# Kernel tuning notes

Hardware: AMD Instinct MI355X
Metric: run time of the kernel (lower is better)

Reference implementation:

```python
import jax, jax.numpy as jnp
import numpy as np


def setup_inputs() -> dict:
    key = jax.random.key(0)
    ks = jax.random.split(key, 4)
    B, T, D, H = 64, 512, 512, 1024
    return {
        "x": jax.random.normal(ks[0], (B, T, D), dtype=jnp.float32),
        "kz": jax.random.normal(ks[1], (D, H), dtype=jnp.float32) * (1.0 / np.sqrt(D)),
        "kr": jax.random.normal(ks[2], (D, H), dtype=jnp.float32) * (1.0 / np.sqrt(D)),
        "kh": jax.random.normal(ks[3], (D, H), dtype=jnp.float32) * (1.0 / np.sqrt(D)),
        "mz": jnp.ones((H,), dtype=jnp.float32),
        "mr": jnp.ones((H,), dtype=jnp.float32),
        "br": jnp.zeros((H,), dtype=jnp.float32),
        "bz": jnp.zeros((H,), dtype=jnp.float32),
    }


def reference(x, kz, kr, kh, mz, mr, br, bz):
    B, T, D = x.shape
    H = kz.shape[1]
    # Precompute input projections for all timesteps (batched GEMMs),
    # identical math to per-step matmuls in the original cell.
    xz = jnp.einsum("btd,dh->bth", x, kz)  # [B,T,H]
    xr = jnp.einsum("btd,dh->bth", x, kr)
    xh = jnp.einsum("btd,dh->bth", x, kh)

    def step(h, inp):
        xz_t, xr_t, xh_t = inp  # each [B,H]
        r = jnp.tanh(xr_t + h * mr + br) + 1.0
        z = jax.nn.sigmoid(xz_t + h * mz + bz)
        h_new = z * h + (1.0 - z) * jnp.tanh(xh_t + r * h)
        return h_new, h_new

    h0 = jnp.zeros((B, H), dtype=x.dtype)
    # scan over time axis: move T to leading dim
    xs = (jnp.swapaxes(xz, 0, 1), jnp.swapaxes(xr, 0, 1), jnp.swapaxes(xh, 0, 1))
    _, ys = jax.lax.scan(step, h0, xs)  # ys: [T,B,H]
    return jnp.swapaxes(ys, 0, 1)  # [B,T,H]
```

## Files before the change

### kernel.cpp

```cpp
#include <hip/hip_runtime.h>
#include <hip/hip_bf16.h>
#include <math.h>


#define M_DIM 32768
#define K_DIM 512
#define H_DIM 1024
#define N3    3072

typedef _Float16 half8v __attribute__((ext_vector_type(8)));
typedef _Float16 half4v __attribute__((ext_vector_type(4)));
typedef float f32x4 __attribute__((ext_vector_type(4)));

__device__ __forceinline__ f32x4 mfma16(half8v a, half8v b, f32x4 c) {
    return __builtin_amdgcn_mfma_f32_16x16x32_f16(a, b, c, 0, 0, 0);
}

__device__ __forceinline__ void load_lds16(const void* g, void* l) {
    __builtin_amdgcn_global_load_lds(
        (const __attribute__((address_space(1))) void*)g,
        (__attribute__((address_space(3))) void*)l, 16, 0, 0);
}

__global__ __launch_bounds__(256) void convert_x(
    const float4* __restrict__ x4, half4v* __restrict__ hi4,
    half4v* __restrict__ lo4, int n4)
{
    int i = blockIdx.x * 256 + threadIdx.x;
    if (i >= n4) return;
    float4 v = x4[i];
    half4v h, lo;
    h.x = (_Float16)v.x; lo.x = (_Float16)(v.x - (float)h.x);
    h.y = (_Float16)v.y; lo.y = (_Float16)(v.y - (float)h.y);
    h.z = (_Float16)v.z; lo.z = (_Float16)(v.z - (float)h.z);
    h.w = (_Float16)v.w; lo.w = (_Float16)(v.w - (float)h.w);
    hi4[i] = h; lo4[i] = lo;
}

__global__ __launch_bounds__(256) void convert_wt(
    const float* __restrict__ kz, const float* __restrict__ kr,
    const float* __restrict__ kh, _Float16* __restrict__ wth,
    _Float16* __restrict__ wtl)
{
    int gid = blockIdx.x * 256 + threadIdx.x;
    int k = gid & (K_DIM - 1);
    int n = (gid >> 9) & (H_DIM - 1);
    int wsel = gid >> 19;
    const float* s = (wsel == 0) ? kz : ((wsel == 1) ? kr : kh);
    float v = s[(size_t)k * H_DIM + n];
    _Float16 h = (_Float16)v;
    wth[gid] = h;
    wtl[gid] = (_Float16)(v - (float)h);
}

__global__ __launch_bounds__(256) void gemm_mfma_split(
    const _Float16* __restrict__ Ahi, const _Float16* __restrict__ Alo,
    const _Float16* __restrict__ Bthi, const _Float16* __restrict__ Btlo,
    float* __restrict__ XZ, float* __restrict__ XR, float* __restrict__ OUT)
{
    __shared__ _Float16 Ah[128 * 32];
    __shared__ _Float16 Al[128 * 32];
    __shared__ _Float16 Bh[128 * 32];
    __shared__ _Float16 Bl[128 * 32];

    const int tid = threadIdx.x;
    const int w = tid >> 6, l = tid & 63;
    const int l15 = l & 15, quad = l >> 4;
    const int bx = blockIdx.x, by = blockIdx.y;
    const long m0 = (long)by * 128;
    const long n0 = (long)bx * 128;

    f32x4 acc[4][4] = {};

    const int s1 = tid, s2 = tid + 256;
    const long aoff1 = (m0 + (s1 >> 2)) * K_DIM + (s1 & 3) * 8;
    const long aoff2 = (m0 + (s2 >> 2)) * K_DIM + (s2 & 3) * 8;
    const long boff1 = (n0 + (s1 >> 2)) * K_DIM + (s1 & 3) * 8;
    const long boff2 = (n0 + (s2 >> 2)) * K_DIM + (s2 & 3) * 8;

    const _Float16* a1 = Ahi + aoff1;  const _Float16* a2 = Ahi + aoff2;
    const _Float16* q1 = Alo + aoff1;  const _Float16* q2 = Alo + aoff2;
    const _Float16* b1 = Bthi + boff1; const _Float16* b2 = Bthi + boff2;
    const _Float16* c1 = Btlo + boff1; const _Float16* c2 = Btlo + boff2;

    _Float16* ldsA1 = &Ah[w * 512]; _Float16* ldsA2 = &Ah[2048 + w * 512];
    _Float16* ldsQ1 = &Al[w * 512]; _Float16* ldsQ2 = &Al[2048 + w * 512];
    _Float16* ldsB1 = &Bh[w * 512]; _Float16* ldsB2 = &Bh[2048 + w * 512];
    _Float16* ldsC1 = &Bl[w * 512]; _Float16* ldsC2 = &Bl[2048 + w * 512];

    const int wm = (w >> 1) * 64, wn = (w & 1) * 64;

    for (int kk = 0; kk < K_DIM / 32; ++kk) {
        load_lds16(a1, ldsA1); load_lds16(a2, ldsA2);
        load_lds16(q1, ldsQ1); load_lds16(q2, ldsQ2);
        load_lds16(b1, ldsB1); load_lds16(b2, ldsB2);
        load_lds16(c1, ldsC1); load_lds16(c2, ldsC2);
        a1 += 32; a2 += 32; q1 += 32; q2 += 32;
        b1 += 32; b2 += 32; c1 += 32; c2 += 32;
        __syncthreads();

        half8v afh[4], afl[4], bfh[4], bfl[4];
#pragma unroll
        for (int mi = 0; mi < 4; ++mi) {
            int row = (wm + mi * 16 + l15) * 32 + quad * 8;
            afh[mi] = *(const half8v*)&Ah[row];
            afl[mi] = *(const half8v*)&Al[row];
        }
#pragma unroll
        for (int ni = 0; ni < 4; ++ni) {
            int row = (wn + ni * 16 + l15) * 32 + quad * 8;
            bfh[ni] = *(const half8v*)&Bh[row];
            bfl[ni] = *(const half8v*)&Bl[row];
        }
#pragma unroll
        for (int mi = 0; mi < 4; ++mi)
#pragma unroll
            for (int ni = 0; ni < 4; ++ni) {
                acc[mi][ni] = mfma16(afh[mi], bfh[ni], acc[mi][ni]);
                acc[mi][ni] = mfma16(afh[mi], bfl[ni], acc[mi][ni]);
                acc[mi][ni] = mfma16(afl[mi], bfh[ni], acc[mi][ni]);
            }
        __syncthreads();
    }

    float* dst = (bx < 8) ? XZ : ((bx < 16) ? XR : OUT);
    const long nl = (long)(bx & 7) * 128 + wn + l15;
#pragma unroll
    for (int mi = 0; mi < 4; ++mi) {
        const long m = m0 + wm + mi * 16 + quad * 4;
#pragma unroll
        for (int ni = 0; ni < 4; ++ni) {
            float* p = dst + m * H_DIM + nl + ni * 16;
#pragma unroll
            for (int i = 0; i < 4; ++i)
                p[(long)i * H_DIM] = acc[mi][ni][i];
        }
    }
}

#define BM 128
#define BN 128
#define BK 8
__global__ __launch_bounds__(256) void gemm_f32(
    const float* __restrict__ A, const float* __restrict__ B,
    float* __restrict__ C, int M, int N, int K)
{
    __shared__ float As[BK][BM];
    __shared__ float Bs[BK][BN];
    const int tid = threadIdx.x;
    const int bm = blockIdx.y * BM, bn = blockIdx.x * BN;
    const int tx = tid & 15, ty = tid >> 4;
    float acc[8][8];
#pragma unroll
    for (int i = 0; i < 8; i++)
#pragma unroll
        for (int j = 0; j < 8; j++) acc[i][j] = 0.f;
    const int a_row = tid >> 1, a_k = (tid & 1) * 4;
    const int b_row = tid >> 5, b_col = (tid & 31) * 4;
    const float* Aptr = A + (size_t)(bm + a_row) * K + a_k;
    const float* Bptr = B + (size_t)b_row * N + bn + b_col;
    for (int k0 = 0; k0 < K; k0 += BK) {
        float4 av = *(const float4*)(Aptr + k0);
        float4 bv = *(const float4*)(Bptr + (size_t)k0 * N);
        As[a_k + 0][a_row] = av.x; As[a_k + 1][a_row] = av.y;
        As[a_k + 2][a_row] = av.z; As[a_k + 3][a_row] = av.w;
        *(float4*)&Bs[b_row][b_col] = bv;
        __syncthreads();
#pragma unroll
        for (int kk = 0; kk < BK; kk++) {
            float4 a0 = *(const float4*)&As[kk][ty * 8];
            float4 a1 = *(const float4*)&As[kk][ty * 8 + 4];
            float4 b0 = *(const float4*)&Bs[kk][tx * 8];
            float4 b1 = *(const float4*)&Bs[kk][tx * 8 + 4];
            float a[8] = {a0.x, a0.y, a0.z, a0.w, a1.x, a1.y, a1.z, a1.w};
            float b[8] = {b0.x, b0.y, b0.z, b0.w, b1.x, b1.y, b1.z, b1.w};
#pragma unroll
            for (int i = 0; i < 8; i++)
#pragma unroll
                for (int j = 0; j < 8; j++)
                    acc[i][j] = fmaf(a[i], b[j], acc[i][j]);
        }
        __syncthreads();
    }
    float* Cptr = C + (size_t)(bm + ty * 8) * N + bn + tx * 8;
#pragma unroll
    for (int i = 0; i < 8; i++) {
        float4 c0 = {acc[i][0], acc[i][1], acc[i][2], acc[i][3]};
        float4 c1 = {acc[i][4], acc[i][5], acc[i][6], acc[i][7]};
        *(float4*)(Cptr + (size_t)i * N)     = c0;
        *(float4*)(Cptr + (size_t)i * N + 4) = c1;
    }
}

__device__ __forceinline__ float fast_tanh(float x) {
    return 1.0f - 2.0f / (__expf(2.0f * x) + 1.0f);
}
__device__ __forceinline__ float fast_sigmoid(float x) {
    return 1.0f / (1.0f + __expf(-x));
}

__global__ __launch_bounds__(256) void scan_kernel(
    const float* __restrict__ XZ, const float* __restrict__ XR,
    float* __restrict__ OUT,
    const float* __restrict__ mz, const float* __restrict__ mr,
    const float* __restrict__ br, const float* __restrict__ bz)
{
    const int gid = blockIdx.x * blockDim.x + threadIdx.x;
    const int b = gid >> 10;
    const int h = gid & (H_DIM - 1);

    const float mzv = mz[h], mrv = mr[h], brv = br[h], bzv = bz[h];
    float hs = 0.f;
    size_t idx = (size_t)b * 512 * H_DIM + h;

    float cz[8], cr[8], ch[8];
#pragma unroll
    for (int j = 0; j < 8; ++j) {
        cz[j] = XZ[idx + (size_t)j * H_DIM];
        cr[j] = XR[idx + (size_t)j * H_DIM];
        ch[j] = OUT[idx + (size_t)j * H_DIM];
    }
    for (int t0 = 0; t0 < 512; t0 += 8) {
        float nz[8], nr[8], nh[8];
        const bool more = (t0 + 8) < 512;
        const size_t nidx = idx + 8ul * H_DIM;
        if (more) {
#pragma unroll
            for (int j = 0; j < 8; ++j) {
                nz[j] = XZ[nidx + (size_t)j * H_DIM];
                nr[j] = XR[nidx + (size_t)j * H_DIM];
                nh[j] = OUT[nidx + (size_t)j * H_DIM];
            }
        }
#pragma unroll
        for (int j = 0; j < 8; ++j) {
            const float r = fast_tanh(fmaf(hs, mrv, cr[j]) + brv) + 1.0f;
            const float z = fast_sigmoid(fmaf(hs, mzv, cz[j]) + bzv);
            const float hn = fmaf(z, hs, (1.0f - z) * fast_tanh(fmaf(r, hs, ch[j])));
            OUT[idx + (size_t)j * H_DIM] = hn;
            hs = hn;
        }
        idx = nidx;
        if (more) {
#pragma unroll
            for (int j = 0; j < 8; ++j) { cz[j] = nz[j]; cr[j] = nr[j]; ch[j] = nh[j]; }
        }
    }
}

extern "C" void kernel_launch(void* const* d_in, const int* in_sizes, int n_in,
                              void* d_out, int out_size, void* d_ws, size_t ws_size,
                              hipStream_t stream) {
    const float* x  = (const float*)d_in[0];
    const float* kz = (const float*)d_in[1];
    const float* kr = (const float*)d_in[2];
    const float* kh = (const float*)d_in[3];
    const float* mz = (const float*)d_in[4];
    const float* mr = (const float*)d_in[5];
    const float* br = (const float*)d_in[6];
    const float* bz = (const float*)d_in[7];
    float* out = (float*)d_out;

    char* ws = (char*)d_ws;
    float* XZ = (float*)ws;
    float* XR = (float*)(ws + 134217728ul);
    _Float16* XHI = (_Float16*)(ws + 268435456ul);
    _Float16* XLO = (_Float16*)(ws + 301989888ul);
    _Float16* WTH = (_Float16*)(ws + 335544320ul);
    _Float16* WTL = (_Float16*)(ws + 338690048ul);
    const size_t need = 341835776ul;

    if (ws_size >= need) {
        int n4 = M_DIM * K_DIM / 4;
        convert_x<<<n4 / 256, 256, 0, stream>>>(
            (const float4*)x, (half4v*)XHI, (half4v*)XLO, n4);
        convert_wt<<<(3 * H_DIM * K_DIM) / 256, 256, 0, stream>>>(
            kz, kr, kh, WTH, WTL);
        dim3 grid(N3 / 128, M_DIM / 128);
        gemm_mfma_split<<<grid, 256, 0, stream>>>(
            XHI, XLO, WTH, WTL, XZ, XR, out);
    } else {
        dim3 grid(H_DIM / BN, M_DIM / BM);
        gemm_f32<<<grid, 256, 0, stream>>>(x, kz, XZ,  M_DIM, H_DIM, K_DIM);
        gemm_f32<<<grid, 256, 0, stream>>>(x, kr, XR,  M_DIM, H_DIM, K_DIM);
        gemm_f32<<<grid, 256, 0, stream>>>(x, kh, out, M_DIM, H_DIM, K_DIM);
    }

    scan_kernel<<<(64 * H_DIM) / 256, 256, 0, stream>>>(
        XZ, XR, out, mz, mr, br, bz);
}
```

Baseline: 645.6 us.

## Stage scan inputs through double-buffered LDS with cooperative float4 loads

The scan kernel now assigns one block per (batch, 256-wide H slice). Threads cooperatively load 8-timestep chunks of XZ, XR and the XH-in-OUT buffer using float4 loads into a double-buffered shared-memory tile. The next chunk is prefetched into registers while the current chunk is computed. This replaces per-thread scalar strided loads with wider coalesced loads and cuts register pressure from the 24-value prefetch arrays. It adds one __syncthreads per chunk and slightly rewrites the h update algebra.

```diff
diff --git a/kernel.cpp b/kernel.cpp
--- a/kernel.cpp
+++ b/kernel.cpp
@@ -192,6 +192,8 @@
     }
 }
 
+#define TC 8
+
 __device__ __forceinline__ float fast_tanh(float x) {
     return 1.0f - 2.0f / (__expf(2.0f * x) + 1.0f);
 }
@@ -205,45 +207,72 @@
     const float* __restrict__ mz, const float* __restrict__ mr,
     const float* __restrict__ br, const float* __restrict__ bz)
 {
-    const int gid = blockIdx.x * blockDim.x + threadIdx.x;
-    const int b = gid >> 10;
-    const int h = gid & (H_DIM - 1);
-
-    const float mzv = mz[h], mrv = mr[h], brv = br[h], bzv = bz[h];
+    __shared__ float lds[2][3][TC][256];
+    float* ldsf = &lds[0][0][0][0];
+
+    const int tid  = threadIdx.x;
+    const int w    = tid >> 6;
+    const int lane = tid & 63;
+    const int b    = blockIdx.x >> 2;
+    const int hblk = blockIdx.x & 3;
+    const int h    = (hblk << 8) | tid;
+
+    const float mzv = mz[h], mrv = mr[h];
+    const float brv = br[h], bzv = bz[h];
+
+    const size_t bbase  = (size_t)b * 512 * H_DIM;
+    const size_t rowoff = (size_t)(hblk << 8) + ((size_t)lane << 2);
+
+    const float* gp[6];
+    int ldsoff[6];
+#pragma unroll
+    for (int i = 0; i < 6; ++i) {
+        const int p = w * 6 + i;
+        const int arr = p >> 3, t = p & 7;
+        const float* base = (arr == 0) ? XZ : ((arr == 1) ? XR : OUT);
+        gp[i] = base + bbase + rowoff + (size_t)t * H_DIM;
+        ldsoff[i] = (arr * TC + t) * 256 + (lane << 2);
+    }
+
+    float4 buf[6];
+#pragma unroll
+    for (int i = 0; i < 6; ++i) buf[i] = *(const float4*)gp[i];
+#pragma unroll
+    for (int i = 0; i < 6; ++i) *(float4*)(ldsf + ldsoff[i]) = buf[i];
+
     float hs = 0.f;
-    size_t idx = (size_t)b * 512 * H_DIM + h;
-
-    float cz[8], cr[8], ch[8];
-#pragma unroll
-    for (int j = 0; j < 8; ++j) {
-        cz[j] = XZ[idx + (size_t)j * H_DIM];
-        cr[j] = XR[idx + (size_t)j * H_DIM];
-        ch[j] = OUT[idx + (size_t)j * H_DIM];
-    }
-    for (int t0 = 0; t0 < 512; t0 += 8) {
-        float nz[8], nr[8], nh[8];
-        const bool more = (t0 + 8) < 512;
-        const size_t nidx = idx + 8ul * H_DIM;
-        if (more) {
-#pragma unroll
-            for (int j = 0; j < 8; ++j) {
-                nz[j] = XZ[nidx + (size_t)j * H_DIM];
-                nr[j] = XR[nidx + (size_t)j * H_DIM];
-                nh[j] = OUT[nidx + (size_t)j * H_DIM];
-            }
-        }
-#pragma unroll
-        for (int j = 0; j < 8; ++j) {
-            const float r = fast_tanh(fmaf(hs, mrv, cr[j]) + brv) + 1.0f;
-            const float z = fast_sigmoid(fmaf(hs, mzv, cz[j]) + bzv);
-            const float hn = fmaf(z, hs, (1.0f - z) * fast_tanh(fmaf(r, hs, ch[j])));
-            OUT[idx + (size_t)j * H_DIM] = hn;
-            hs = hn;
-        }
-        idx = nidx;
-        if (more) {
-#pragma unroll
-            for (int j = 0; j < 8; ++j) { cz[j] = nz[j]; cr[j] = nr[j]; ch[j] = nh[j]; }
+    size_t oidx = bbase + h;
+
+    for (int c = 0; c < 512 / TC; ++c) {
+        __syncthreads();
+        const int q = c & 1;
+        if (c < 512 / TC - 1) {
+            const size_t adv = (size_t)(c + 1) * TC * H_DIM;
+#pragma unroll
+            for (int i = 0; i < 6; ++i)
+                buf[i] = *(const float4*)(gp[i] + adv);
+        }
+        float vz[TC], vr[TC], vh[TC];
+#pragma unroll
+        for (int t = 0; t < TC; ++t) {
+            vz[t] = lds[q][0][t][tid] + bzv;
+            vr[t] = lds[q][1][t][tid] + brv;
+            vh[t] = lds[q][2][t][tid];
+        }
+#pragma unroll
+        for (int t = 0; t < TC; ++t) {
+            const float r  = fast_tanh(fmaf(hs, mrv, vr[t])) + 1.0f;
+            const float z  = fast_sigmoid(fmaf(hs, mzv, vz[t]));
+            const float th = fast_tanh(fmaf(r, hs, vh[t]));
+            hs = fmaf(z, hs - th, th);
+            OUT[oidx] = hs;
+            oidx += H_DIM;
+        }
+        if (c < 512 / TC - 1) {
+            float* dstbase = ldsf + ((c + 1) & 1) * (3 * TC * 256);
+#pragma unroll
+            for (int i = 0; i < 6; ++i)
+                *(float4*)(dstbase + ldsoff[i]) = buf[i];
         }
     }
 }
```

After: 696.6 us. +7.9%, slower.
